# Kernel tuning notes

Measured on AMD Instinct MI355X. Metric: run time of the kernel, lower is better.

Reference implementation:

```python
import jax, jax.numpy as jnp
import numpy as np

DIM = 3072
NUM_HEADS = 24
HEAD_DIM = 128
SEQ = 2048
BATCH = 1
EPS = 1e-6


def _make_rope(seq_len: int, head_dim: int):
    # Standard RoPE angles; cos/sin laid out per interleaved-pair convention
    # (each frequency repeated for the (real, imag) pair), shape [S, head_dim].
    half = head_dim // 2
    inv_freq = 1.0 / (10000.0 ** (np.arange(0, half, dtype=np.float32) / half))
    t = np.arange(seq_len, dtype=np.float32)
    freqs = np.outer(t, inv_freq)  # [S, half]
    freqs = np.repeat(freqs, 2, axis=-1)  # [S, head_dim], pairs share the angle
    return jnp.asarray(np.cos(freqs)), jnp.asarray(np.sin(freqs))


def setup_inputs() -> dict:
    key = jax.random.key(0)
    ks = jax.random.split(key, 8)
    inner = NUM_HEADS * HEAD_DIM
    s = 0.02
    hidden_states = jax.random.normal(ks[0], (BATCH, SEQ, DIM), dtype=jnp.float32)
    wq = jax.random.normal(ks[1], (inner, DIM), dtype=jnp.float32) * s
    wk = jax.random.normal(ks[2], (inner, DIM), dtype=jnp.float32) * s
    wv = jax.random.normal(ks[3], (inner, DIM), dtype=jnp.float32) * s
    bq = jax.random.normal(ks[4], (inner,), dtype=jnp.float32) * s
    bk = jax.random.normal(ks[5], (inner,), dtype=jnp.float32) * s
    bv = jax.random.normal(ks[6], (inner,), dtype=jnp.float32) * s
    norm_q_w = jnp.ones((HEAD_DIM,), dtype=jnp.float32)
    norm_k_w = jnp.ones((HEAD_DIM,), dtype=jnp.float32)
    cos, sin = _make_rope(SEQ, HEAD_DIM)
    return {
        "hidden_states": hidden_states,
        "wq": wq, "bq": bq, "wk": wk, "bk": bk, "wv": wv, "bv": bv,
        "norm_q_w": norm_q_w, "norm_k_w": norm_k_w,
        "cos": cos, "sin": sin,
    }


def _rms_norm(x, w, eps=EPS):
    # RMSNorm over the last (head_dim) axis.
    var = jnp.mean(jnp.square(x), axis=-1, keepdims=True)
    return x * jax.lax.rsqrt(var + eps) * w


def _apply_rope(x, cos, sin):
    # x: [B, S, H, D]; cos/sin: [S, D]. Interleaved-pair rotation
    # (diffusers apply_rotary_emb, use_real_unbind_dim=-1).
    xr = x[..., 0::2]
    xi = x[..., 1::2]
    rot = jnp.stack([-xi, xr], axis=-1).reshape(x.shape)
    c = cos[None, :, None, :]
    s = sin[None, :, None, :]
    return x * c + rot * s


def reference(hidden_states, wq, bq, wk, bk, wv, bv, norm_q_w, norm_k_w, cos, sin):
    B, S, _ = hidden_states.shape
    H, D = NUM_HEADS, HEAD_DIM
    # QKV projections (ColumnParallelLinear with tp_size=1)
    q = (hidden_states @ wq.T + bq).reshape(B, S, H, D)
    k = (hidden_states @ wk.T + bk).reshape(B, S, H, D)
    v = (hidden_states @ wv.T + bv).reshape(B, S, H, D)
    # qk-norm then RoPE
    q = _apply_rope(_rms_norm(q, norm_q_w), cos, sin)
    k = _apply_rope(_rms_norm(k, norm_k_w), cos, sin)
    # Non-causal full attention
    scale = 1.0 / jnp.sqrt(jnp.asarray(D, dtype=q.dtype))
    scores = jnp.einsum("bqhd,bkhd->bhqk", q, k) * scale
    probs = jax.nn.softmax(scores, axis=-1)
    out = jnp.einsum("bhqk,bkhd->bqhd", probs, v)
    return out.reshape(B, S, H * D).astype(q.dtype)
```

## Files before the change

kernel.cpp:

```cpp
#include <hip/hip_runtime.h>

#define S_LEN 2048
#define DIMSZ 3072
#define NHEAD 24
#define HDIM 128
#define NQKV 9216
#define QSCALE 0.08838834764831845f
#define FMAX 12.0f

typedef unsigned short u16;
typedef unsigned int u32;
typedef __attribute__((ext_vector_type(8))) short short8;
typedef __attribute__((ext_vector_type(4))) float f32x4;

__device__ __forceinline__ u16 f2bf(float f) {
    u32 u = __float_as_uint(f);
    u32 r = (u + 0x7fffu + ((u >> 16) & 1u)) >> 16;
    return (u16)r;
}
__device__ __forceinline__ float bf2f(u16 u) {
    return __uint_as_float((u32)u << 16);
}
__device__ __forceinline__ u32 cvtpk_bf16(float lo, float hi) {
    u32 r;
    asm("v_cvt_pk_bf16_f32 %0, %1, %2" : "=v"(r) : "v"(lo), "v"(hi));
    return r;
}

__device__ __forceinline__ void lds16(u16* lds, const u16* g) {
    __builtin_amdgcn_global_load_lds((const __attribute__((address_space(1))) u32*)g,
                                     (__attribute__((address_space(3))) u32*)lds, 16, 0, 0);
}

__global__ void k_conv(const float4* __restrict__ hs, const float4* __restrict__ wq,
                       const float4* __restrict__ wk, const float4* __restrict__ wv,
                       u16* __restrict__ hs_b, u16* __restrict__ w_b) {
    int i = blockIdx.x * 256 + threadIdx.x;
    const float4* src;
    u16* dst;
    if (i < 1572864) { src = hs + i; dst = hs_b + (size_t)i * 4; }
    else if (i < 3932160) { src = wq + (i - 1572864); dst = w_b + (size_t)(i - 1572864) * 4; }
    else if (i < 6291456) { src = wk + (i - 3932160); dst = w_b + 9437184 + (size_t)(i - 3932160) * 4; }
    else { src = wv + (i - 6291456); dst = w_b + 18874368 + (size_t)(i - 6291456) * 4; }
    float4 v = *src;
    u32 lo = (u32)f2bf(v.x) | ((u32)f2bf(v.y) << 16);
    u32 hi = (u32)f2bf(v.z) | ((u32)f2bf(v.w) << 16);
    uint2 p; p.x = lo; p.y = hi;
    *(uint2*)dst = p;
}

__global__ __launch_bounds__(256, 2) void k_gemm(const u16* __restrict__ A, const u16* __restrict__ W,
                                                 u16* __restrict__ C) {
    __shared__ __align__(16) u16 As[2][256 * 32];
    __shared__ __align__(16) u16 Bs[2][192 * 32];
    const int tid = threadIdx.x, wave = tid >> 6, lane = tid & 63;
    const int bm = blockIdx.x & 7, bn = blockIdx.x >> 3;
    const int frow = lane & 15, fk = lane >> 4;
    const u16* baseA = A + (size_t)(bm * 256) * DIMSZ;

    auto stageA = [&](int b, int kt) {
#pragma unroll
        for (int j = 0; j < 4; ++j) {
            int flat = j * 256 + tid, row = flat >> 2, ch = flat & 3;
            lds16(&As[b][flat * 8], baseA + (size_t)row * DIMSZ + kt * 32 + ((ch ^ ((row >> 1) & 3)) * 8));
        }
    };
    auto stageB = [&](int b, int kt) {
#pragma unroll
        for (int j = 0; j < 3; ++j) {
            int flat = j * 256 + tid, row = flat >> 2, ch = flat & 3;
            int srow = bn * 144 + row;
            srow = (srow > NQKV - 1) ? (NQKV - 1) : srow;
            lds16(&Bs[b][flat * 8], W + (size_t)srow * DIMSZ + kt * 32 + ((ch ^ ((row >> 1) & 3)) * 8));
        }
    };

    stageA(0, 0); stageB(0, 0); stageA(1, 1); stageB(1, 1);
    asm volatile("s_waitcnt vmcnt(7)");
    __builtin_amdgcn_s_barrier();

    f32x4 acc[4][9] = {};
    for (int T = 0; T < 96; ++T) {
        const int b = T & 1;
        const u16* LA = As[b];
        const u16* LB = Bs[b];
        short8 af[4], bf[9];
#pragma unroll
        for (int mf = 0; mf < 4; ++mf) {
            int row = wave * 64 + mf * 16 + frow;
            af[mf] = *(const short8*)&LA[row * 32 + ((fk ^ ((row >> 1) & 3)) * 8)];
        }
#pragma unroll
        for (int nf = 0; nf < 9; ++nf) {
            int row = nf * 16 + frow;
            bf[nf] = *(const short8*)&LB[row * 32 + ((fk ^ ((row >> 1) & 3)) * 8)];
        }
        __builtin_amdgcn_s_setprio(1);
#pragma unroll
        for (int mf = 0; mf < 4; ++mf)
#pragma unroll
            for (int nf = 0; nf < 9; ++nf)
                acc[mf][nf] = __builtin_amdgcn_mfma_f32_16x16x32_bf16(af[mf], bf[nf], acc[mf][nf], 0, 0, 0);
        __builtin_amdgcn_s_setprio(0);
        __builtin_amdgcn_s_barrier();
        if (T < 94) {
            stageA(b, T + 2); stageB(b, T + 2);
            asm volatile("s_waitcnt vmcnt(7)");
            __builtin_amdgcn_s_barrier();
        } else if (T == 94) {
            asm volatile("s_waitcnt vmcnt(0)");
            __builtin_amdgcn_s_barrier();
        }
    }

#pragma unroll
    for (int mf = 0; mf < 4; ++mf) {
#pragma unroll
        for (int nf = 0; nf < 9; ++nf) {
            int n = bn * 144 + nf * 16 + frow;
#pragma unroll
            for (int i = 0; i < 4; ++i) {
                int m = bm * 256 + wave * 64 + mf * 16 + fk * 4 + i;
                C[(size_t)m * NQKV + n] = f2bf(acc[mf][nf][i]);
            }
        }
    }
}

__global__ void k_post(const u16* __restrict__ qkv, const float* __restrict__ nw_q,
                       const float* __restrict__ nw_k, const float* __restrict__ bq,
                       const float* __restrict__ bk, const float* __restrict__ bv,
                       const float* __restrict__ cosT, const float* __restrict__ sinT,
                       u16* __restrict__ Qb, u16* __restrict__ Kb, u16* __restrict__ Vt) {
    const int tid = threadIdx.x;
    const int row = blockIdx.x * 16 + (tid >> 4);
    const int lane16 = tid & 15;
    const int s = row & 2047, h = row >> 11;
    const int d0 = lane16 * 8;
    const u16* base = qkv + (size_t)s * NQKV + h * HDIM + d0;

    float cs[8], sn[8];
    *(float4*)&cs[0] = *(const float4*)&cosT[s * HDIM + d0];
    *(float4*)&cs[4] = *(const float4*)&cosT[s * HDIM + d0 + 4];
    *(float4*)&sn[0] = *(const float4*)&sinT[s * HDIM + d0];
    *(float4*)&sn[4] = *(const float4*)&sinT[s * HDIM + d0 + 4];

    {
        short8 raw = *(const short8*)base;
        float b[8];
        *(float4*)&b[0] = *(const float4*)&bq[h * HDIM + d0];
        *(float4*)&b[4] = *(const float4*)&bq[h * HDIM + d0 + 4];
        float x[8], ss = 0.f;
#pragma unroll
        for (int j = 0; j < 8; ++j) { x[j] = bf2f((u16)raw[j]) + b[j]; ss += x[j] * x[j]; }
#pragma unroll
        for (int m = 1; m < 16; m <<= 1) ss += __shfl_xor(ss, m);
        float r = rsqrtf(ss * (1.0f / 128.0f) + 1e-6f);
        float w[8];
        *(float4*)&w[0] = *(const float4*)&nw_q[d0];
        *(float4*)&w[4] = *(const float4*)&nw_q[d0 + 4];
        u32 pk[4];
#pragma unroll
        for (int jp = 0; jp < 4; ++jp) {
            float e = x[2 * jp] * r * w[2 * jp];
            float o = x[2 * jp + 1] * r * w[2 * jp + 1];
            float y0 = (e * cs[2 * jp] - o * sn[2 * jp]) * QSCALE;
            float y1 = (o * cs[2 * jp] + e * sn[2 * jp]) * QSCALE;
            pk[jp] = cvtpk_bf16(y0, y1);
        }
        uint4 v; v.x = pk[0]; v.y = pk[1]; v.z = pk[2]; v.w = pk[3];
        *(uint4*)&Qb[((size_t)h * S_LEN + s) * HDIM + d0] = v;
    }
    {
        short8 raw = *(const short8*)(base + 3072);
        float b[8];
        *(float4*)&b[0] = *(const float4*)&bk[h * HDIM + d0];
        *(float4*)&b[4] = *(const float4*)&bk[h * HDIM + d0 + 4];
        float x[8], ss = 0.f;
#pragma unroll
        for (int j = 0; j < 8; ++j) { x[j] = bf2f((u16)raw[j]) + b[j]; ss += x[j] * x[j]; }
#pragma unroll
        for (int m = 1; m < 16; m <<= 1) ss += __shfl_xor(ss, m);
        float r = rsqrtf(ss * (1.0f / 128.0f) + 1e-6f);
        float w[8];
        *(float4*)&w[0] = *(const float4*)&nw_k[d0];
        *(float4*)&w[4] = *(const float4*)&nw_k[d0 + 4];
        u32 pk[4];
#pragma unroll
        for (int jp = 0; jp < 4; ++jp) {
            float e = x[2 * jp] * r * w[2 * jp];
            float o = x[2 * jp + 1] * r * w[2 * jp + 1];
            float y0 = e * cs[2 * jp] - o * sn[2 * jp];
            float y1 = o * cs[2 * jp] + e * sn[2 * jp];
            pk[jp] = cvtpk_bf16(y0, y1);
        }
        uint4 v; v.x = pk[0]; v.y = pk[1]; v.z = pk[2]; v.w = pk[3];
        *(uint4*)&Kb[((size_t)h * S_LEN + s) * HDIM + d0] = v;
    }
    {
        short8 raw = *(const short8*)(base + 6144);
        float b[8];
        *(float4*)&b[0] = *(const float4*)&bv[h * HDIM + d0];
        *(float4*)&b[4] = *(const float4*)&bv[h * HDIM + d0 + 4];
#pragma unroll
        for (int j = 0; j < 8; ++j)
            Vt[((size_t)h * HDIM + d0 + j) * S_LEN + s] = f2bf(bf2f((u16)raw[j]) + b[j]);
    }
}

__global__ __launch_bounds__(128, 2) void k_attn(const u16* __restrict__ Qb, const u16* __restrict__ Kb,
                                                 const u16* __restrict__ Vt, float* __restrict__ out) {
    __shared__ __align__(16) u16 Ks[2][32 * 128];
    __shared__ __align__(16) u16 Vs[2][128 * 32];
    __shared__ __align__(16) u16 Ps[2][32 * 32];
    const int tid = threadIdx.x;
    const int wave = tid >> 6, lane = tid & 63;
    const int wg = (blockIdx.x & 7) * 96 + (blockIdx.x >> 3);
    const int h = wg >> 5, qb = wg & 31;
    const int frow = lane & 15, fk = lane >> 4;

    short8 qf[2][4];
#pragma unroll
    for (int qg = 0; qg < 2; ++qg) {
        const u16* qbase = Qb + ((size_t)h * S_LEN + qb * 64 + wave * 32 + qg * 16 + frow) * HDIM + fk * 8;
#pragma unroll
        for (int ks = 0; ks < 4; ++ks) qf[qg][ks] = *(const short8*)(qbase + ks * 32);
    }

    f32x4 o[2][8] = {};
    float l_p[2] = {0.f, 0.f};

#define STAGE(buf, kt)                                                                        \
    {                                                                                         \
        _Pragma("unroll") for (int c = 0; c < 4; ++c) {                                       \
            int flat = c * 128 + tid;                                                         \
            int r = flat >> 4, ch = flat & 15;                                                \
            lds16(Ks[buf] + flat * 8,                                                         \
                  Kb + ((size_t)h * S_LEN + (kt) * 32 + r) * HDIM + ((ch ^ (r & 15)) * 8));   \
        }                                                                                     \
        _Pragma("unroll") for (int c = 0; c < 4; ++c) {                                       \
            int flat = c * 128 + tid;                                                         \
            int r = flat >> 2, ch = flat & 3;                                                 \
            lds16(Vs[buf] + flat * 8,                                                         \
                  Vt + ((size_t)h * HDIM + r) * S_LEN + (kt) * 32 + ((ch ^ ((r >> 2) & 3)) * 8)); \
        }                                                                                     \
    }

    STAGE(0, 0);
    __syncthreads();
    int cur = 0;

    for (int kt = 0; kt < 64; ++kt) {
        if (kt + 1 < 64) STAGE(cur ^ 1, kt + 1);
        f32x4 sacc[2][2] = {};
        __builtin_amdgcn_s_setprio(1);
#pragma unroll
        for (int nf = 0; nf < 2; ++nf) {
#pragma unroll
            for (int ks = 0; ks < 4; ++ks) {
                short8 kf = *(const short8*)&Ks[cur][(nf * 16 + frow) * 128 + (((ks * 4 + fk) ^ frow) * 8)];
#pragma unroll
                for (int qg = 0; qg < 2; ++qg)
                    sacc[qg][nf] = __builtin_amdgcn_mfma_f32_16x16x32_bf16(kf, qf[qg][ks], sacc[qg][nf], 0, 0, 0);
            }
        }
        __builtin_amdgcn_s_setprio(0);
#pragma unroll
        for (int qg = 0; qg < 2; ++qg) {
            int prow = qg * 16 + frow;
#pragma unroll
            for (int nf = 0; nf < 2; ++nf) {
                float p0 = __expf(sacc[qg][nf][0] - FMAX);
                float p1 = __expf(sacc[qg][nf][1] - FMAX);
                float p2 = __expf(sacc[qg][nf][2] - FMAX);
                float p3 = __expf(sacc[qg][nf][3] - FMAX);
                l_p[qg] += (p0 + p1) + (p2 + p3);
                uint2 pk;
                pk.x = cvtpk_bf16(p0, p1);
                pk.y = cvtpk_bf16(p2, p3);
                int c16 = (nf * 2 + (fk >> 1)) ^ ((prow >> 2) & 3);
                *(uint2*)&Ps[wave][prow * 32 + c16 * 8 + (fk & 1) * 4] = pk;
            }
        }
        short8 pf[2];
#pragma unroll
        for (int qg = 0; qg < 2; ++qg)
            pf[qg] = *(const short8*)&Ps[wave][(qg * 16 + frow) * 32 + ((fk ^ ((frow >> 2) & 3)) * 8)];
        __builtin_amdgcn_s_setprio(1);
#pragma unroll
        for (int nf8 = 0; nf8 < 8; ++nf8) {
            short8 vf = *(const short8*)&Vs[cur][(nf8 * 16 + frow) * 32 + ((fk ^ ((frow >> 2) & 3)) * 8)];
#pragma unroll
            for (int qg = 0; qg < 2; ++qg)
                o[qg][nf8] = __builtin_amdgcn_mfma_f32_16x16x32_bf16(pf[qg], vf, o[qg][nf8], 0, 0, 0);
        }
        __builtin_amdgcn_s_setprio(0);
        __syncthreads();
        cur ^= 1;
    }
#undef STAGE

#pragma unroll
    for (int qg = 0; qg < 2; ++qg) {
        l_p[qg] += __shfl_xor(l_p[qg], 16);
        l_p[qg] += __shfl_xor(l_p[qg], 32);
    }

#pragma unroll
    for (int qg = 0; qg < 2; ++qg)
#pragma unroll
        for (int i = 0; i < 4; ++i) {
            float rinv = 1.0f / __shfl(l_p[qg], fk * 4 + i);
            int srow = qb * 64 + wave * 32 + qg * 16 + fk * 4 + i;
#pragma unroll
            for (int nf8 = 0; nf8 < 8; ++nf8)
                out[(size_t)srow * DIMSZ + h * HDIM + nf8 * 16 + frow] = o[qg][nf8][i] * rinv;
        }
}

extern "C" void kernel_launch(void* const* d_in, const int* in_sizes, int n_in,
                              void* d_out, int out_size, void* d_ws, size_t ws_size,
                              hipStream_t stream) {
    const float* hs = (const float*)d_in[0];
    const float* wq = (const float*)d_in[1];
    const float* bq = (const float*)d_in[2];
    const float* wk = (const float*)d_in[3];
    const float* bk = (const float*)d_in[4];
    const float* wv = (const float*)d_in[5];
    const float* bv = (const float*)d_in[6];
    const float* nq = (const float*)d_in[7];
    const float* nk = (const float*)d_in[8];
    const float* cosT = (const float*)d_in[9];
    const float* sinT = (const float*)d_in[10];
    float* out = (float*)d_out;

    char* ws = (char*)d_ws;
    u16* hs_b = (u16*)(ws);
    u16* w_b = (u16*)(ws + 12582912);
    u16* qkv = (u16*)(ws + 69206016);
    u16* Qb = (u16*)(ws + 106954752);
    u16* Kb = (u16*)(ws + 119537664);
    u16* Vt = (u16*)(ws + 132120576);

    k_conv<<<dim3(33792), 256, 0, stream>>>((const float4*)hs, (const float4*)wq,
                                            (const float4*)wk, (const float4*)wv, hs_b, w_b);

    k_gemm<<<dim3(512), 256, 0, stream>>>(hs_b, w_b, qkv);

    k_post<<<dim3(3072), 256, 0, stream>>>(qkv, nq, nk, bq, bk, bv, cosT, sinT, Qb, Kb, Vt);

    k_attn<<<dim3(768), 128, 0, stream>>>(Qb, Kb, Vt, out);
}
```

Baseline: 287.1 us.

## Load K/V fragments directly from global memory instead of LDS staging

Removes the double-buffered LDS staging of K and V tiles and the per-iteration block barrier. Each wave now loads its MFMA operand fragments directly from global memory every iteration. This drops the LDS write/read and synchronisation cost but duplicates global loads across the two waves. It also loses the explicit prefetch of the next tile, so memory latency may be exposed.

```diff
diff --git a/kernel.cpp b/kernel.cpp
--- a/kernel.cpp
+++ b/kernel.cpp
@@ -210,8 +210,6 @@
 
 __global__ __launch_bounds__(128, 2) void k_attn(const u16* __restrict__ Qb, const u16* __restrict__ Kb,
                                                  const u16* __restrict__ Vt, float* __restrict__ out) {
-    __shared__ __align__(16) u16 Ks[2][32 * 128];
-    __shared__ __align__(16) u16 Vs[2][128 * 32];
     __shared__ __align__(16) u16 Ps[2][32 * 32];
     const int tid = threadIdx.x;
     const int wave = tid >> 6, lane = tid & 63;
@@ -227,44 +225,35 @@
         for (int ks = 0; ks < 4; ++ks) qf[qg][ks] = *(const short8*)(qbase + ks * 32);
     }
 
+    const u16* Kbase = Kb + (size_t)h * S_LEN * HDIM;
+    const u16* Vbase = Vt + (size_t)h * HDIM * S_LEN;
+
     f32x4 o[2][8] = {};
     float l_p[2] = {0.f, 0.f};
 
-#define STAGE(buf, kt)                                                                        \
-    {                                                                                         \
-        _Pragma("unroll") for (int c = 0; c < 4; ++c) {                                       \
-            int flat = c * 128 + tid;                                                         \
-            int r = flat >> 4, ch = flat & 15;                                                \
-            lds16(Ks[buf] + flat * 8,                                                         \
-                  Kb + ((size_t)h * S_LEN + (kt) * 32 + r) * HDIM + ((ch ^ (r & 15)) * 8));   \
-        }                                                                                     \
-        _Pragma("unroll") for (int c = 0; c < 4; ++c) {                                       \
-            int flat = c * 128 + tid;                                                         \
-            int r = flat >> 2, ch = flat & 3;                                                 \
-            lds16(Vs[buf] + flat * 8,                                                         \
-                  Vt + ((size_t)h * HDIM + r) * S_LEN + (kt) * 32 + ((ch ^ ((r >> 2) & 3)) * 8)); \
-        }                                                                                     \
-    }
-
-    STAGE(0, 0);
-    __syncthreads();
-    int cur = 0;
-
     for (int kt = 0; kt < 64; ++kt) {
-        if (kt + 1 < 64) STAGE(cur ^ 1, kt + 1);
+        short8 kf[2][4];
+#pragma unroll
+        for (int nf = 0; nf < 2; ++nf)
+#pragma unroll
+            for (int ks = 0; ks < 4; ++ks)
+                kf[nf][ks] = *(const short8*)&Kbase[(size_t)(kt * 32 + nf * 16 + frow) * HDIM + (ks * 4 + fk) * 8];
+        short8 vf[8];
+#pragma unroll
+        for (int nf8 = 0; nf8 < 8; ++nf8)
+            vf[nf8] = *(const short8*)&Vbase[(size_t)(nf8 * 16 + frow) * S_LEN + kt * 32 + fk * 8];
+
         f32x4 sacc[2][2] = {};
         __builtin_amdgcn_s_setprio(1);
 #pragma unroll
-        for (int nf = 0; nf < 2; ++nf) {
-#pragma unroll
-            for (int ks = 0; ks < 4; ++ks) {
-                short8 kf = *(const short8*)&Ks[cur][(nf * 16 + frow) * 128 + (((ks * 4 + fk) ^ frow) * 8)];
+        for (int nf = 0; nf < 2; ++nf)
+#pragma unroll
+            for (int ks = 0; ks < 4; ++ks)
 #pragma unroll
                 for (int qg = 0; qg < 2; ++qg)
-                    sacc[qg][nf] = __builtin_amdgcn_mfma_f32_16x16x32_bf16(kf, qf[qg][ks], sacc[qg][nf], 0, 0, 0);
-            }
-        }
+                    sacc[qg][nf] = __builtin_amdgcn_mfma_f32_16x16x32_bf16(kf[nf][ks], qf[qg][ks], sacc[qg][nf], 0, 0, 0);
         __builtin_amdgcn_s_setprio(0);
+
 #pragma unroll
         for (int qg = 0; qg < 2; ++qg) {
             int prow = qg * 16 + frow;
@@ -288,17 +277,12 @@
             pf[qg] = *(const short8*)&Ps[wave][(qg * 16 + frow) * 32 + ((fk ^ ((frow >> 2) & 3)) * 8)];
         __builtin_amdgcn_s_setprio(1);
 #pragma unroll
-        for (int nf8 = 0; nf8 < 8; ++nf8) {
-            short8 vf = *(const short8*)&Vs[cur][(nf8 * 16 + frow) * 32 + ((fk ^ ((frow >> 2) & 3)) * 8)];
+        for (int nf8 = 0; nf8 < 8; ++nf8)
 #pragma unroll
             for (int qg = 0; qg < 2; ++qg)
-                o[qg][nf8] = __builtin_amdgcn_mfma_f32_16x16x32_bf16(pf[qg], vf, o[qg][nf8], 0, 0, 0);
-        }
+                o[qg][nf8] = __builtin_amdgcn_mfma_f32_16x16x32_bf16(pf[qg], vf[nf8], o[qg][nf8], 0, 0, 0);
         __builtin_amdgcn_s_setprio(0);
-        __syncthreads();
-        cur ^= 1;
-    }
-#undef STAGE
+    }
 
 #pragma unroll
     for (int qg = 0; qg < 2; ++qg) {
```

New measurement: 372.3 us. 29.6% more time.
